# Kernel optimization log

Hardware: AMD Instinct MI355X
Metric: run time of the kernel (lower is better)

## Reference

```python
import jax, jax.numpy as jnp
import numpy as np

BEV_H = 200
BEV_W = 200
H_METERS = 100.0
W_METERS = 100.0
THRESHOLD = 0.05
LOW_PASS = 0.3  # 3DGS screen-space low-pass filter added to cov2D diagonal
ALPHA_MIN = 1.0 / 255.0
ALPHA_MAX = 0.99


def setup_inputs() -> dict:
    key = jax.random.key(0)
    k1, k2, k3, k4 = jax.random.split(key, 4)
    B, G, D = 2, 2000, 32
    features = jax.random.normal(k1, (B, G, D), dtype=jnp.float32)
    # means uniformly covering the [-50, 50] x [-50, 50] BEV extent (z unused)
    means3D = (jax.random.uniform(k2, (B, G, 3), dtype=jnp.float32) - 0.5) * 100.0
    # PSD 3x3 covariances, ~1-2 m std -> a few pixels at 2 px/m
    A = jax.random.normal(k3, (B, G, 3, 3), dtype=jnp.float32)
    Sigma = jnp.einsum('bgij,bgkj->bgik', A, A) + 0.1 * jnp.eye(3, dtype=jnp.float32)
    iu = jnp.triu_indices(3)
    cov3D = Sigma[:, :, iu[0], iu[1]]  # b g 6 : (xx, xy, xz, yy, yz, zz)
    opacities = jax.random.uniform(k4, (B, G, 1), dtype=jnp.float32)
    return {'features': features, 'means3D': means3D, 'cov3D': cov3D,
            'opacities': opacities}


def _render(features, means3D, cov3D, opacities):
    B, G, D = features.shape
    sh = BEV_H / H_METERS  # 2 px / m
    sw = BEV_W / W_METERS
    op = opacities[..., 0]                      # b g
    mask = op > THRESHOLD                       # opacity gating (torch masks rows;
                                                # zero-alpha is mathematically identical)
    # orthographic BEV projection (full_proj_transform rows 0 and 1)
    x, y = means3D[..., 0], means3D[..., 1]
    u = -sh * y + BEV_H / 2.0                   # row coordinate, b g
    v = -sw * x + BEV_W / 2.0                   # col coordinate, b g
    # cov2D = M Sigma M^T with M = [[0, sh, 0], [sw, 0, 0]], plus low-pass
    sxx, sxy, syy = cov3D[..., 0], cov3D[..., 1], cov3D[..., 3]
    c00 = sh * sh * syy + LOW_PASS
    c01 = sh * sw * sxy
    c11 = sw * sw * sxx + LOW_PASS
    det = c00 * c11 - c01 * c01
    valid = mask & (det > 0.0)
    inv_det = jnp.where(det > 0.0, 1.0 / jnp.where(det > 0.0, det, 1.0), 0.0)
    cA = c11 * inv_det                          # conic (A, B, C)
    cB = -c01 * inv_det
    cC = c00 * inv_det
    # per-pixel Gaussian power, separably broadcast: [b g H 1] + [b g 1 W]
    gi = jnp.arange(BEV_H, dtype=jnp.float32)
    gj = jnp.arange(BEV_W, dtype=jnp.float32)
    du = u[..., None] - gi                      # b g H
    dv = v[..., None] - gj                      # b g W
    power = (-0.5 * cA)[..., None, None] * (du * du)[..., :, None] \
          + (-0.5 * cC)[..., None, None] * (dv * dv)[..., None, :] \
          + (-cB)[..., None, None] * du[..., :, None] * dv[..., None, :]  # b g H W
    alpha = jnp.minimum(ALPHA_MAX, op[..., None, None] * jnp.exp(power))
    keep = valid[..., None, None] & (power <= 0.0) & (alpha >= ALPHA_MIN)
    alpha = jnp.where(keep, alpha, 0.0)
    alpha = alpha.reshape(B, G, BEV_H * BEV_W)  # b g p
    # front-to-back alpha compositing: exclusive cumprod of transmittance
    T_excl = jnp.concatenate(
        [jnp.ones((B, 1, BEV_H * BEV_W), dtype=alpha.dtype),
         jnp.cumprod(1.0 - alpha, axis=1)[:, :-1]], axis=1)
    weight = alpha * T_excl                     # b g p
    out = jnp.einsum('bgp,bgd->bdp', weight, features)  # bg_color is zeros
    out = out.reshape(B, D, BEV_H, BEV_W)
    num_gaussians = jnp.mean(jnp.sum(mask.astype(jnp.float32), axis=1))
    return out, num_gaussians


def reference(features, means3D, cov3D, opacities):
    return _render(features, means3D, cov3D, opacities)
```

## Files before the change

### kernel.cpp

```cpp
#include <hip/hip_runtime.h>
#include <math.h>

#define BEV_H 200
#define BEV_W 200
#define NPIX (BEV_H * BEV_W)
#define TILE 8
#define NT 25
#define NB 2
#define T_DEAD 1e-10f
#define SEGCAP 512
#define PCAP 128
#define KC 32
#define NLOG255 (-5.5412635f)

__device__ __forceinline__ unsigned pk2bf(float x, float y)
{
    unsigned ux = __float_as_uint(x), uy = __float_as_uint(y);
    ux = ux + 0x7fffu + ((ux >> 16) & 1u);
    uy = uy + 0x7fffu + ((uy >> 16) & 1u);
    return (ux >> 16) | (uy & 0xffff0000u);
}

__global__ __launch_bounds__(256, 5) void render_fused_kernel(
    const float* __restrict__ features, const float* __restrict__ means3D,
    const float* __restrict__ cov3D, const float* __restrict__ opac,
    float* __restrict__ out, int G)
{
    __shared__ __align__(16) unsigned char smem[24576];
    unsigned short* glist = (unsigned short*)smem;
    float4* plA = (float4*)(smem + 4096);
    float2* plB = (float2*)(smem + 12288);
    uint4*  flq = (uint4*)(smem + 16384);
    float*  xch = (float*)smem;

    const int tid  = threadIdx.x;
    const int lane = tid & 63;
    const int w    = tid >> 6;
    const int b  = blockIdx.z;
    const int tj = blockIdx.x;
    const int ti = blockIdx.y;
    const int j = tj * TILE + (lane & 7);
    const int i = ti * TILE + (lane >> 3);
    const float fi = (float)i, fj = (float)j;
    const float ti_lo = (float)(ti * TILE), ti_hi = ti_lo + (TILE - 1);
    const float tj_lo = (float)(tj * TILE), tj_hi = tj_lo + (TILE - 1);
    const int gbase = b * G;
    const int g_lo = (w * G) >> 2;
    const int g_hi = ((w + 1) * G) >> 2;
    const int rounds = (g_hi - g_lo + 63) >> 6;

    int tot = 0;
    {
        int gg = min(g_lo + lane, g_hi - 1);
        size_t gi = (size_t)(gbase + gg);
        float x0 = means3D[gi * 3 + 0], y0 = means3D[gi * 3 + 1];
        float s0 = cov3D[gi * 6 + 0], s1 = cov3D[gi * 6 + 1], s3 = cov3D[gi * 6 + 3];
        float o0 = opac[gi];
        for (int r = 0; r < rounds; ++r) {
            float x1 = 0.f, y1 = 0.f, t0 = 0.f, t1 = 0.f, t3 = 0.f, o1 = 0.f;
            if (r + 1 < rounds) {
                const int gn = min(g_lo + (r + 1) * 64 + lane, g_hi - 1);
                const size_t gni = (size_t)(gbase + gn);
                x1 = means3D[gni * 3 + 0]; y1 = means3D[gni * 3 + 1];
                t0 = cov3D[gni * 6 + 0];   t1 = cov3D[gni * 6 + 1];
                t3 = cov3D[gni * 6 + 3];   o1 = opac[gni];
            }
            const int g = g_lo + r * 64 + lane;
            const float u = -2.0f * y0 + 100.0f;
            const float v = -2.0f * x0 + 100.0f;
            const float c00 = 4.0f * s3 + 0.3f;
            const float c01 = 4.0f * s1;
            const float c11 = 4.0f * s0 + 0.3f;
            const float det = c00 * c11 - c01 * c01;
            bool keep = false;
            float L = 0.0f;
            if (o0 > 0.05f && det > 0.0f && g < g_hi) {
                L = __logf(255.0f * o0);
                const float tl2 = 2.0f * L;
                const float dut = fmaxf(fmaxf(ti_lo - u, u - ti_hi), 0.0f);
                const float dvt = fmaxf(fmaxf(tj_lo - v, v - tj_hi), 0.0f);
                keep = (dut * dut <= tl2 * c00 + 1e-4f) &&
                       (dvt * dvt <= tl2 * c11 + 1e-4f);
            }
            const unsigned long long bal = __ballot(keep);
            if (keep) {
                const int slot = tot + (int)__popcll(bal & ((1ull << lane) - 1ull));
                glist[w * SEGCAP + slot] = (unsigned short)g;
                if (slot < PCAP) {
                    const float inv = 1.0f / det;
                    plA[w * PCAP + slot] =
                        make_float4(u, v, -0.5f * c11 * inv, c01 * inv);
                    plB[w * PCAP + slot] = make_float2(-0.5f * c00 * inv,
                                                       L + NLOG255);
                }
            }
            tot += (int)__popcll(bal);
            x0 = x1; y0 = y1; s0 = t0; s1 = t1; s3 = t3; o0 = o1;
        }
    }

    float acc[32];
#pragma unroll
    for (int d = 0; d < 32; ++d) acc[d] = 0.0f;
    float T = 1.0f;

    for (int k0 = 0; k0 < tot; k0 += KC) {
        if (!__any(T >= T_DEAD)) break;
        const int nk = min(KC, tot - k0);

        if (k0 >= PCAP && lane < nk) {
            const int g = glist[w * SEGCAP + k0 + lane];
            const size_t gi = (size_t)(gbase + g);
            const float x = means3D[gi * 3 + 0], y = means3D[gi * 3 + 1];
            const float sxx = cov3D[gi * 6 + 0], sxy = cov3D[gi * 6 + 1],
                        syy = cov3D[gi * 6 + 3];
            const float op = opac[gi];
            const float u = -2.0f * y + 100.0f;
            const float v = -2.0f * x + 100.0f;
            const float c00 = 4.0f * syy + 0.3f;
            const float c01 = 4.0f * sxy;
            const float c11 = 4.0f * sxx + 0.3f;
            const float inv = 1.0f / (c00 * c11 - c01 * c01);
            plA[w * PCAP + lane] = make_float4(u, v, -0.5f * c11 * inv, c01 * inv);
            plB[w * PCAP + lane] = make_float2(-0.5f * c00 * inv, __logf(op));
        }
        for (int idx = lane; idx < nk * 4; idx += 64) {
            const int e = idx >> 2, q = idx & 3;
            const int g = glist[w * SEGCAP + k0 + e];
            const float4* fp =
                (const float4*)(features + (size_t)(gbase + g) * 32) + q * 2;
            const float4 A = fp[0], Bq = fp[1];
            flq[(w * KC + e) * 4 + q] =
                make_uint4(pk2bf(A.x, A.y), pk2bf(A.z, A.w),
                           pk2bf(Bq.x, Bq.y), pk2bf(Bq.z, Bq.w));
        }

        const int pbase = w * PCAP + ((k0 < PCAP) ? k0 : 0);
        for (int k = 0; k < nk; ++k) {
            const float4 pA = plA[pbase + k];
            const float2 pB = plB[pbase + k];
            const float du = pA.x - fi;
            const float dv = pA.y - fj;
            const float power = pA.z * du * du + pB.x * dv * dv + pA.w * du * dv;
            const float powb = power + pB.y;
            float alpha = fminf(0.99f, __expf(powb));
            const bool ok = (powb >= NLOG255) && (power <= 0.0f);
            alpha = ok ? alpha : 0.0f;
            const float wgt = alpha * T;
            T *= 1.0f - alpha;
#pragma unroll
            for (int q = 0; q < 4; ++q) {
                const uint4 uq = flq[(w * KC + k) * 4 + q];
                const unsigned uu[4] = {uq.x, uq.y, uq.z, uq.w};
#pragma unroll
                for (int c = 0; c < 4; ++c) {
                    const float lof = __uint_as_float(uu[c] << 16);
                    const float hif = __uint_as_float(uu[c] & 0xffff0000u);
                    acc[q * 8 + c * 2 + 0] = fmaf(wgt, lof, acc[q * 8 + c * 2 + 0]);
                    acc[q * 8 + c * 2 + 1] = fmaf(wgt, hif, acc[q * 8 + c * 2 + 1]);
                }
            }
        }
    }

    __syncthreads();
    if (w != 0) {
        float* row = xch + ((w - 1) * 64 + lane) * 17;
        unsigned* urow = (unsigned*)row;
#pragma unroll
        for (int c2 = 0; c2 < 16; ++c2)
            urow[c2] = pk2bf(acc[2 * c2], acc[2 * c2 + 1]);
        row[16] = T;
    }
    __syncthreads();

    if (w == 0) {
        float W = T;
#pragma unroll
        for (int r = 1; r <= 3; ++r) {
            const float* row = xch + ((r - 1) * 64 + lane) * 17;
            const unsigned* urow = (const unsigned*)row;
#pragma unroll
            for (int c2 = 0; c2 < 16; ++c2) {
                const unsigned uv = urow[c2];
                acc[2 * c2 + 0] = fmaf(W, __uint_as_float(uv << 16),
                                       acc[2 * c2 + 0]);
                acc[2 * c2 + 1] = fmaf(W, __uint_as_float(uv & 0xffff0000u),
                                       acc[2 * c2 + 1]);
            }
            W *= row[16];
        }

        const int p = i * BEV_W + j;
        float* ob = out + (size_t)b * 32 * NPIX + p;
#pragma unroll
        for (int d = 0; d < 32; ++d) ob[(size_t)d * NPIX] = acc[d];
    }

    if (w == 1 && blockIdx.x == 0 && blockIdx.y == 0 && blockIdx.z == 0) {
        const float4* o4 = (const float4*)opac;
        const int n4 = (NB * G) >> 2;
        float s = 0.0f;
        for (int idx = lane; idx < n4; idx += 64) {
            const float4 o = o4[idx];
            s += (o.x > 0.05f ? 1.0f : 0.0f) + (o.y > 0.05f ? 1.0f : 0.0f) +
                 (o.z > 0.05f ? 1.0f : 0.0f) + (o.w > 0.05f ? 1.0f : 0.0f);
        }
#pragma unroll
        for (int off = 32; off > 0; off >>= 1) s += __shfl_down(s, off);
        if (lane == 0) out[NB * 32 * NPIX] = s * (1.0f / NB);
    }
}

extern "C" void kernel_launch(void* const* d_in, const int* in_sizes, int n_in,
                              void* d_out, int out_size, void* d_ws, size_t ws_size,
                              hipStream_t stream)
{
    const float* features = (const float*)d_in[0];
    const float* means3D  = (const float*)d_in[1];
    const float* cov3D    = (const float*)d_in[2];
    const float* opac     = (const float*)d_in[3];
    float* out = (float*)d_out;

    const int G = in_sizes[3] / NB;

    dim3 grid(NT, NT, NB);
    render_fused_kernel<<<grid, 256, 0, stream>>>(features, means3D, cov3D, opac,
                                                  out, G);
}
```

Measured before the change: 81.41 us.

## Precompute per-Gaussian conics, tile bounds and bf16 features in a prep kernel

Adds a prep kernel that computes, once per Gaussian, the projected conic parameters, the row and column tile-index bounds, and bf16-packed features, and stores them in workspace. The render kernel then culls each tile with integer range checks on the bounds and copies the precomputed records into shared memory. Previously all 1250 tile blocks recomputed the projection and culling math and repacked features from scratch. The cost is an extra kernel launch plus a global round-trip. The culling loop is also hardcoded to 8 rounds of 64, with a stride of 2048, which assumes G is small.

```diff
diff --git a/kernel.cpp b/kernel.cpp
--- a/kernel.cpp
+++ b/kernel.cpp
@@ -12,6 +12,12 @@
 #define PCAP 128
 #define KC 32
 #define NLOG255 (-5.5412635f)
+#define GSTRIDE 2048
+
+#define WS_PPA 0
+#define WS_PPB (WS_PPA + NB * GSTRIDE * 16)
+#define WS_BND (WS_PPB + NB * GSTRIDE * 8)
+#define WS_PF  (WS_BND + NB * GSTRIDE * 4)
 
 __device__ __forceinline__ unsigned pk2bf(float x, float y)
 {
@@ -21,9 +27,69 @@
     return (ux >> 16) | (uy & 0xffff0000u);
 }
 
-__global__ __launch_bounds__(256, 5) void render_fused_kernel(
+__global__ __launch_bounds__(256) void prep_kernel(
     const float* __restrict__ features, const float* __restrict__ means3D,
     const float* __restrict__ cov3D, const float* __restrict__ opac,
+    float4* __restrict__ ppA, float2* __restrict__ ppB,
+    unsigned* __restrict__ bnd, uint4* __restrict__ pf, int G)
+{
+    const int t = blockIdx.x * 256 + threadIdx.x;
+
+    if (t < NB * GSTRIDE) {
+        const int b = t >> 11;
+        const int g = t & (GSTRIDE - 1);
+        unsigned bd = 0x000000FFu;
+        if (g < G) {
+            const size_t gi = (size_t)(b * G + g);
+            const float x = means3D[gi * 3 + 0], y = means3D[gi * 3 + 1];
+            const float s0 = cov3D[gi * 6 + 0], s1 = cov3D[gi * 6 + 1],
+                        s3 = cov3D[gi * 6 + 3];
+            const float op = opac[gi];
+            const float u = -2.0f * y + 100.0f;
+            const float v = -2.0f * x + 100.0f;
+            const float c00 = 4.0f * s3 + 0.3f;
+            const float c01 = 4.0f * s1;
+            const float c11 = 4.0f * s0 + 0.3f;
+            const float det = c00 * c11 - c01 * c01;
+            if (op > 0.05f && det > 0.0f) {
+                const float L = __logf(255.0f * op);
+                const float Au = 2.0f * L * c00 + 1e-4f;
+                const float Av = 2.0f * L * c11 + 1e-4f;
+                int ti0 = 255, ti1 = 0, tj0 = 255, tj1 = 0;
+                for (int tt = 0; tt < NT; ++tt) {
+                    const float lo = (float)(tt * TILE), hi = lo + (TILE - 1);
+                    const float dut = fmaxf(fmaxf(lo - u, u - hi), 0.0f);
+                    const float dvt = fmaxf(fmaxf(lo - v, v - hi), 0.0f);
+                    if (dut * dut <= Au) { if (tt < ti0) ti0 = tt; ti1 = tt; }
+                    if (dvt * dvt <= Av) { if (tt < tj0) tj0 = tt; tj1 = tt; }
+                }
+                const float inv = 1.0f / det;
+                ppA[t] = make_float4(u, v, -0.5f * c11 * inv, c01 * inv);
+                ppB[t] = make_float2(-0.5f * c00 * inv, L + NLOG255);
+                bd = (unsigned)ti0 | ((unsigned)ti1 << 8) |
+                     ((unsigned)tj0 << 16) | ((unsigned)tj1 << 24);
+            }
+        }
+        bnd[t] = bd;
+    }
+
+    if (t < NB * G * 4) {
+        const int q = t & 3;
+        const int gg = t >> 2;
+        const int b = (gg >= G) ? 1 : 0;
+        const int g = gg - b * G;
+        const float4* fp = (const float4*)(features + (size_t)gg * 32) + q * 2;
+        const float4 A = fp[0], Bq = fp[1];
+        pf[(size_t)(b * GSTRIDE + g) * 4 + q] =
+            make_uint4(pk2bf(A.x, A.y), pk2bf(A.z, A.w),
+                       pk2bf(Bq.x, Bq.y), pk2bf(Bq.z, Bq.w));
+    }
+}
+
+__global__ __launch_bounds__(256, 5) void render_fused_kernel(
+    const float* __restrict__ opac,
+    const float4* __restrict__ ppA, const float2* __restrict__ ppB,
+    const unsigned* __restrict__ bndg, const uint4* __restrict__ pf,
     float* __restrict__ out, int G)
 {
     __shared__ __align__(16) unsigned char smem[24576];
@@ -42,60 +108,34 @@
     const int j = tj * TILE + (lane & 7);
     const int i = ti * TILE + (lane >> 3);
     const float fi = (float)i, fj = (float)j;
-    const float ti_lo = (float)(ti * TILE), ti_hi = ti_lo + (TILE - 1);
-    const float tj_lo = (float)(tj * TILE), tj_hi = tj_lo + (TILE - 1);
-    const int gbase = b * G;
     const int g_lo = (w * G) >> 2;
     const int g_hi = ((w + 1) * G) >> 2;
-    const int rounds = (g_hi - g_lo + 63) >> 6;
+    const int pbase0 = b * GSTRIDE;
 
     int tot = 0;
     {
-        int gg = min(g_lo + lane, g_hi - 1);
-        size_t gi = (size_t)(gbase + gg);
-        float x0 = means3D[gi * 3 + 0], y0 = means3D[gi * 3 + 1];
-        float s0 = cov3D[gi * 6 + 0], s1 = cov3D[gi * 6 + 1], s3 = cov3D[gi * 6 + 3];
-        float o0 = opac[gi];
-        for (int r = 0; r < rounds; ++r) {
-            float x1 = 0.f, y1 = 0.f, t0 = 0.f, t1 = 0.f, t3 = 0.f, o1 = 0.f;
-            if (r + 1 < rounds) {
-                const int gn = min(g_lo + (r + 1) * 64 + lane, g_hi - 1);
-                const size_t gni = (size_t)(gbase + gn);
-                x1 = means3D[gni * 3 + 0]; y1 = means3D[gni * 3 + 1];
-                t0 = cov3D[gni * 6 + 0];   t1 = cov3D[gni * 6 + 1];
-                t3 = cov3D[gni * 6 + 3];   o1 = opac[gni];
-            }
+        unsigned bv[8];
+        const unsigned* bb = bndg + pbase0 + g_lo;
+#pragma unroll
+        for (int r = 0; r < 8; ++r)
+            bv[r] = bb[r * 64 + lane];
+#pragma unroll
+        for (int r = 0; r < 8; ++r) {
             const int g = g_lo + r * 64 + lane;
-            const float u = -2.0f * y0 + 100.0f;
-            const float v = -2.0f * x0 + 100.0f;
-            const float c00 = 4.0f * s3 + 0.3f;
-            const float c01 = 4.0f * s1;
-            const float c11 = 4.0f * s0 + 0.3f;
-            const float det = c00 * c11 - c01 * c01;
-            bool keep = false;
-            float L = 0.0f;
-            if (o0 > 0.05f && det > 0.0f && g < g_hi) {
-                L = __logf(255.0f * o0);
-                const float tl2 = 2.0f * L;
-                const float dut = fmaxf(fmaxf(ti_lo - u, u - ti_hi), 0.0f);
-                const float dvt = fmaxf(fmaxf(tj_lo - v, v - tj_hi), 0.0f);
-                keep = (dut * dut <= tl2 * c00 + 1e-4f) &&
-                       (dvt * dvt <= tl2 * c11 + 1e-4f);
-            }
+            const unsigned bd = bv[r];
+            const bool keep = (g < g_hi) &&
+                (ti >= (int)(bd & 255u)) && (ti <= (int)((bd >> 8) & 255u)) &&
+                (tj >= (int)((bd >> 16) & 255u)) && (tj <= (int)(bd >> 24));
             const unsigned long long bal = __ballot(keep);
             if (keep) {
                 const int slot = tot + (int)__popcll(bal & ((1ull << lane) - 1ull));
                 glist[w * SEGCAP + slot] = (unsigned short)g;
                 if (slot < PCAP) {
-                    const float inv = 1.0f / det;
-                    plA[w * PCAP + slot] =
-                        make_float4(u, v, -0.5f * c11 * inv, c01 * inv);
-                    plB[w * PCAP + slot] = make_float2(-0.5f * c00 * inv,
-                                                       L + NLOG255);
+                    plA[w * PCAP + slot] = ppA[pbase0 + g];
+                    plB[w * PCAP + slot] = ppB[pbase0 + g];
                 }
             }
             tot += (int)__popcll(bal);
-            x0 = x1; y0 = y1; s0 = t0; s1 = t1; s3 = t3; o0 = o1;
         }
     }
 
@@ -110,29 +150,13 @@
 
         if (k0 >= PCAP && lane < nk) {
             const int g = glist[w * SEGCAP + k0 + lane];
-            const size_t gi = (size_t)(gbase + g);
-            const float x = means3D[gi * 3 + 0], y = means3D[gi * 3 + 1];
-            const float sxx = cov3D[gi * 6 + 0], sxy = cov3D[gi * 6 + 1],
-                        syy = cov3D[gi * 6 + 3];
-            const float op = opac[gi];
-            const float u = -2.0f * y + 100.0f;
-            const float v = -2.0f * x + 100.0f;
-            const float c00 = 4.0f * syy + 0.3f;
-            const float c01 = 4.0f * sxy;
-            const float c11 = 4.0f * sxx + 0.3f;
-            const float inv = 1.0f / (c00 * c11 - c01 * c01);
-            plA[w * PCAP + lane] = make_float4(u, v, -0.5f * c11 * inv, c01 * inv);
-            plB[w * PCAP + lane] = make_float2(-0.5f * c00 * inv, __logf(op));
+            plA[w * PCAP + lane] = ppA[pbase0 + g];
+            plB[w * PCAP + lane] = ppB[pbase0 + g];
         }
         for (int idx = lane; idx < nk * 4; idx += 64) {
             const int e = idx >> 2, q = idx & 3;
             const int g = glist[w * SEGCAP + k0 + e];
-            const float4* fp =
-                (const float4*)(features + (size_t)(gbase + g) * 32) + q * 2;
-            const float4 A = fp[0], Bq = fp[1];
-            flq[(w * KC + e) * 4 + q] =
-                make_uint4(pk2bf(A.x, A.y), pk2bf(A.z, A.w),
-                           pk2bf(Bq.x, Bq.y), pk2bf(Bq.z, Bq.w));
+            flq[(w * KC + e) * 4 + q] = pf[(size_t)(pbase0 + g) * 4 + q];
         }
 
         const int pbase = w * PCAP + ((k0 < PCAP) ? k0 : 0);
@@ -224,7 +248,16 @@
 
     const int G = in_sizes[3] / NB;
 
+    char* ws = (char*)d_ws;
+    float4*   ppA = (float4*)(ws + WS_PPA);
+    float2*   ppB = (float2*)(ws + WS_PPB);
+    unsigned* bnd = (unsigned*)(ws + WS_BND);
+    uint4*    pf  = (uint4*)(ws + WS_PF);
+
+    prep_kernel<<<64, 256, 0, stream>>>(features, means3D, cov3D, opac,
+                                        ppA, ppB, bnd, pf, G);
+
     dim3 grid(NT, NT, NB);
-    render_fused_kernel<<<grid, 256, 0, stream>>>(features, means3D, cov3D, opac,
+    render_fused_kernel<<<grid, 256, 0, stream>>>(opac, ppA, ppB, bnd, pf,
                                                   out, G);
 }
```

Result: no change. 79.89 us (-1.9%).
